# Kernel optimization log

Hardware: AMD Instinct MI355X
Metric: run time of the kernel (lower is better)

## Reference

```python
import jax, jax.numpy as jnp
import numpy as np

R_MAX = 1.0
BASIS_MASK = 0xFF        # low 8 bits -> basis index (basis_size=256)
R_BITS_MASK = 0xFFFF     # next 16 bits -> quantized radius
R_DENOM = 65535.0
INT8_DENOM = 127.0


def setup_inputs() -> dict:
    key = jax.random.key(0)
    k_x, k_c, k_b, k_r, k_s, k_bias = jax.random.split(key, 6)
    B, S, D_in, D_out, BASIS = 4, 2048, 4096, 4096, 256
    x = jax.random.normal(k_x, (B, S, D_in), dtype=jnp.float32)
    codes = jax.random.randint(k_c, (D_out,), 0, 16777216, dtype=jnp.int32)
    basis_table = jax.random.normal(k_b, (BASIS, D_in), dtype=jnp.float32)
    residual_q = jax.random.randint(k_r, (D_out, D_in), 0, 256, dtype=jnp.int32)
    residual_scales = jax.random.uniform(k_s, (D_out,), dtype=jnp.float32) * 0.05
    bias = jax.random.normal(k_bias, (D_out,), dtype=jnp.float32)
    return {"x": x, "codes": codes, "basis_table": basis_table,
            "residual_q": residual_q, "residual_scales": residual_scales,
            "bias": bias}


def decode_weight(codes, basis_table, residual_q, residual_scales):
    # Bitfield decode: low 8 bits = basis index, next 16 bits = quantized radius in [0, r_max].
    idx = codes & BASIS_MASK                                   # [O]
    r = ((codes >> 8) & R_BITS_MASK).astype(jnp.float32) / R_DENOM * R_MAX  # [O]
    base = r[:, None] * basis_table[idx]                       # [O, I]
    resid = (residual_q.astype(jnp.float32) - 128.0) / INT8_DENOM  # dequant int8 residual
    return base + residual_scales[:, None] * resid             # [O, I]


def reference(x, codes, basis_table, residual_q, residual_scales, bias):
    W = decode_weight(codes, basis_table, residual_q, residual_scales)  # [O, I]
    # y = x @ W^T + bias  (fused dequant-matmul in the original CUDA kernel)
    return jnp.einsum("bsi,oi->bso", x, W) + bias
```

## Files before the change

kernel.cpp:

```cpp
#include <hip/hip_runtime.h>


typedef __bf16 bf16x8 __attribute__((ext_vector_type(8)));
typedef float f32x4 __attribute__((ext_vector_type(4)));
typedef int i32x4 __attribute__((ext_vector_type(4)));
typedef unsigned short u16x8 __attribute__((ext_vector_type(8)));

__device__ __forceinline__ unsigned short f2bf(float f) {
    union { float f; unsigned int u; } c; c.f = f;
    unsigned int u = c.u;
    u += 0x7fffu + ((u >> 16) & 1u);
    return (unsigned short)(u >> 16);
}
__device__ __forceinline__ float bf2f(unsigned short h) {
    union { unsigned int u; float f; } c; c.u = ((unsigned int)h) << 16;
    return c.f;
}

__device__ __forceinline__ void load_lds16(const void* g, void* l) {
    __builtin_amdgcn_global_load_lds(
        (__attribute__((address_space(1))) void*)(void*)g,
        (__attribute__((address_space(3))) void*)l,
        16, 0, 0);
}

__device__ __forceinline__ int swz_decode(int p, int row_bytes) {
    const int g = p >> 3, t = p & 7, v = t ^ (g & 7);
    const int row = g * 2 + (v >> 2), chunk = v & 3;
    return row * row_bytes + chunk * 16;
}

__global__ void cvt_bf16_kernel(const float4* __restrict__ in4,
                                ushort4* __restrict__ out4, int n4) {
    int i = blockIdx.x * blockDim.x + threadIdx.x;
    const int stride = gridDim.x * blockDim.x;
    for (; i < n4; i += stride) {
        float4 v = in4[i];
        ushort4 o;
        o.x = f2bf(v.x); o.y = f2bf(v.y); o.z = f2bf(v.z); o.w = f2bf(v.w);
        out4[i] = o;
    }
}

__global__ void quant_x_kernel(const float* __restrict__ x,
                               signed char* __restrict__ xq,
                               float* __restrict__ arow, int K) {
    const int m = blockIdx.x;
    const float* row = x + (size_t)m * K;
    const int base = threadIdx.x * 16;
    float4 v[4];
#pragma unroll
    for (int j = 0; j < 4; ++j) v[j] = *(const float4*)(row + base + j * 4);

    float lmax = 0.f;
#pragma unroll
    for (int j = 0; j < 4; ++j) {
        lmax = fmaxf(lmax, fabsf(v[j].x));
        lmax = fmaxf(lmax, fabsf(v[j].y));
        lmax = fmaxf(lmax, fabsf(v[j].z));
        lmax = fmaxf(lmax, fabsf(v[j].w));
    }
#pragma unroll
    for (int off = 32; off; off >>= 1)
        lmax = fmaxf(lmax, __shfl_xor(lmax, off));
    __shared__ float smax[4];
    if ((threadIdx.x & 63) == 0) smax[threadIdx.x >> 6] = lmax;
    __syncthreads();
    const float mx = fmaxf(fmaxf(smax[0], smax[1]), fmaxf(smax[2], smax[3]));
    const float inv = mx > 0.f ? 127.0f / mx : 0.0f;
    if (threadIdx.x == 0) arow[m] = mx * (1.0f / 127.0f);

    union { signed char c[16]; i32x4 w; } pk;
#pragma unroll
    for (int j = 0; j < 4; ++j) {
        pk.c[j * 4 + 0] = (signed char)(int)rintf(v[j].x * inv);
        pk.c[j * 4 + 1] = (signed char)(int)rintf(v[j].y * inv);
        pk.c[j * 4 + 2] = (signed char)(int)rintf(v[j].z * inv);
        pk.c[j * 4 + 3] = (signed char)(int)rintf(v[j].w * inv);
    }
    *(i32x4*)(xq + (size_t)m * K + base) = pk.w;
}

__global__ void pack_q_kernel(const int4* __restrict__ q4,
                              unsigned int* __restrict__ out, int n4) {
    const int i = blockIdx.x * blockDim.x + threadIdx.x;
    if (i >= n4) return;
    int4 a = q4[i];
    unsigned int w = ((unsigned)(a.x - 128) & 0xFFu)
                   | (((unsigned)(a.y - 128) & 0xFFu) << 8)
                   | (((unsigned)(a.z - 128) & 0xFFu) << 16)
                   | (((unsigned)(a.w - 128) & 0xFFu) << 24);
    out[i] = w;
}

__global__ __launch_bounds__(512) void
p_gemm_kernel(const float* __restrict__ x,
              const unsigned short* __restrict__ Bb,
              unsigned short* __restrict__ Pbf,
              int M, int K) {
    __shared__ __align__(16) float As[2][32 * 64];
    __shared__ __align__(16) unsigned short Bs[2][256 * 64];

    const int tid  = threadIdx.x;
    const int lane = tid & 63;
    const int wv   = tid >> 6;
    const int wr   = wv >> 2;
    const int wc   = wv & 3;
    const int m0 = blockIdx.x * 32;
    const int lr = lane & 15;
    const int kg = lane >> 4;

    f32x4 acc[4];
#pragma unroll
    for (int ni = 0; ni < 4; ++ni) acc[ni] = (f32x4){0.f, 0.f, 0.f, 0.f};

    const int aRow = tid >> 4;
    const int aSrc = (tid & 15) ^ (aRow & 15);
    int bRow[4], bSrc[4];
#pragma unroll
    for (int j = 0; j < 4; ++j) {
        const int p = tid + 512 * j;
        bRow[j] = p >> 3;
        bSrc[j] = (p & 7) ^ (bRow[j] & 7);
    }
    const float* aG = x + (size_t)(m0 + aRow) * K + aSrc * 4;
    const unsigned short* bG[4];
#pragma unroll
    for (int j = 0; j < 4; ++j) bG[j] = Bb + (size_t)bRow[j] * K + bSrc[j] * 8;

#define P_STAGE(bb, k0)                                                        \
    do {                                                                       \
        load_lds16(aG + (k0), (char*)As[bb] + tid * 16);                       \
        _Pragma("unroll") for (int j = 0; j < 4; ++j)                          \
            load_lds16(bG[j] + (k0), (char*)Bs[bb] + (tid + 512 * j) * 16);    \
    } while (0)

    P_STAGE(0, 0);
    const int NT = K >> 6;
    for (int t = 0; t < NT; ++t) {
        const int bb = t & 1;
        if (t + 1 < NT) {
            P_STAGE(bb ^ 1, (t + 1) << 6);
            asm volatile("s_waitcnt vmcnt(5)" ::: "memory");
        } else {
            asm volatile("s_waitcnt vmcnt(0)" ::: "memory");
        }
        __builtin_amdgcn_s_barrier();

        const float* Ab = As[bb];
        const unsigned short* Bbf = Bs[bb];
#pragma unroll
        for (int s = 0; s < 2; ++s) {
            const int r = wr * 16 + lr;
            const int c0 = s * 8 + kg * 2;
            const int ph0 = c0 ^ (r & 15);
            const int ph1 = (c0 + 1) ^ (r & 15);
            f32x4 lo = *(const f32x4*)(Ab + r * 64 + ph0 * 4);
            f32x4 hi = *(const f32x4*)(Ab + r * 64 + ph1 * 4);
            bf16x8 a;
            a[0] = (__bf16)lo[0]; a[1] = (__bf16)lo[1];
            a[2] = (__bf16)lo[2]; a[3] = (__bf16)lo[3];
            a[4] = (__bf16)hi[0]; a[5] = (__bf16)hi[1];
            a[6] = (__bf16)hi[2]; a[7] = (__bf16)hi[3];
#pragma unroll
            for (int ni = 0; ni < 4; ++ni) {
                const int rb = wc * 64 + ni * 16 + lr;
                const int ph = (s * 4 + kg) ^ (rb & 7);
                bf16x8 bfr = __builtin_bit_cast(bf16x8,
                    *(const u16x8*)(Bbf + rb * 64 + ph * 8));
                acc[ni] = __builtin_amdgcn_mfma_f32_16x16x32_bf16(
                    a, bfr, acc[ni], 0, 0, 0);
            }
        }
        __builtin_amdgcn_s_barrier();
    }
#undef P_STAGE

#pragma unroll
    for (int ni = 0; ni < 4; ++ni) {
        const int n = wc * 64 + ni * 16 + lr;
        const int mb = m0 + wr * 16 + kg * 4;
#pragma unroll
        for (int rg = 0; rg < 4; ++rg)
            Pbf[(size_t)(mb + rg) * 256 + n] = f2bf(acc[ni][rg]);
    }
}

__global__ __launch_bounds__(256, 2) void
gemm_i8_kernel(const signed char* __restrict__ Xq,
               const signed char* __restrict__ Qb,
               const float* __restrict__ arow,
               const int* __restrict__ codes,
               const float* __restrict__ scales,
               const float* __restrict__ bias,
               const unsigned short* __restrict__ Pbf,
               float* __restrict__ out,
               int M, int N, int K) {
    __shared__ __align__(16) signed char As[2][128 * 64];
    __shared__ __align__(16) signed char Bs[2][256 * 64];

    const int tid  = threadIdx.x;
    const int lane = tid & 63;
    const int wv   = tid >> 6;
    const int wr   = wv >> 1;
    const int wc   = wv & 1;
    const int m0 = blockIdx.x * 128;
    const int n0 = blockIdx.y * 256;
    const int lr = lane & 15;
    const int kg = lane >> 4;
    const int cidx = (((lr & 1) << 2) | kg) ^ ((lr >> 1) & 7);

    i32x4 acc[4][8];
#pragma unroll
    for (int mi = 0; mi < 4; ++mi)
#pragma unroll
        for (int ni = 0; ni < 8; ++ni)
            acc[mi][ni] = (i32x4){0, 0, 0, 0};

    int gaOff[2], gbOff[4];
#pragma unroll
    for (int j = 0; j < 2; ++j) gaOff[j] = swz_decode(tid + 256 * j, 64);
#pragma unroll
    for (int j = 0; j < 4; ++j) gbOff[j] = swz_decode(tid + 256 * j, 64);

    const signed char* aSrc[2];
    const signed char* bSrc[4];
#pragma unroll
    for (int j = 0; j < 2; ++j)
        aSrc[j] = Xq + (size_t)(m0 + (gaOff[j] >> 6)) * K + (gaOff[j] & 63);
#pragma unroll
    for (int j = 0; j < 4; ++j)
        bSrc[j] = Qb + (size_t)(n0 + (gbOff[j] >> 6)) * K + (gbOff[j] & 63);

#define G_STAGE(bb, k0)                                                        \
    do {                                                                       \
        _Pragma("unroll") for (int j = 0; j < 2; ++j)                          \
            load_lds16(aSrc[j] + (k0), (char*)As[bb] + (tid + 256 * j) * 16);  \
        _Pragma("unroll") for (int j = 0; j < 4; ++j)                          \
            load_lds16(bSrc[j] + (k0), (char*)Bs[bb] + (tid + 256 * j) * 16);  \
    } while (0)

    G_STAGE(0, 0);
    asm volatile("s_waitcnt vmcnt(0)" ::: "memory");
    __builtin_amdgcn_s_barrier();

    const int NT = K >> 6;
#pragma unroll 2
    for (int t = 0; t < NT; ++t) {
        const int bb = t & 1;
        if (t + 1 < NT) G_STAGE(bb ^ 1, (t + 1) << 6);

        i32x4 af[4], bfr[8];
#pragma unroll
        for (int mi = 0; mi < 4; ++mi) {
            const int r2 = wr * 32 + mi * 8 + (lr >> 1);
            af[mi] = *(const i32x4*)(As[bb] + r2 * 128 + cidx * 16);
        }
#pragma unroll
        for (int ni = 0; ni < 8; ++ni) {
            const int r2 = wc * 64 + ni * 8 + (lr >> 1);
            bfr[ni] = *(const i32x4*)(Bs[bb] + r2 * 128 + cidx * 16);
        }
#pragma unroll
        for (int mi = 0; mi < 4; ++mi)
#pragma unroll
            for (int ni = 0; ni < 8; ++ni)
                acc[mi][ni] = __builtin_amdgcn_mfma_i32_16x16x64_i8(
                    af[mi], bfr[ni], acc[mi][ni], 0, 0, 0);

        asm volatile("s_waitcnt vmcnt(0)" ::: "memory");
        __builtin_amdgcn_s_barrier();
    }
#undef G_STAGE

    float av[4][4];
#pragma unroll
    for (int mi = 0; mi < 4; ++mi)
#pragma unroll
        for (int rg = 0; rg < 4; ++rg)
            av[mi][rg] = arow[m0 + wr * 64 + mi * 16 + kg * 4 + rg];

#pragma unroll
    for (int ni = 0; ni < 8; ++ni) {
        const int n = n0 + wc * 128 + ni * 16 + lr;
        const int code = codes[n];
        const int cc = code & 0xFF;
        const float rr = (float)((code >> 8) & 0xFFFF) * (1.0f / 65535.0f);
        const float so = scales[n] * (1.0f / 127.0f);
        const float bv = bias[n];
#pragma unroll
        for (int mi = 0; mi < 4; ++mi) {
            const int mbase = m0 + wr * 64 + mi * 16 + kg * 4;
            unsigned short pv[4];
#pragma unroll
            for (int rg = 0; rg < 4; ++rg)
                pv[rg] = Pbf[(size_t)(mbase + rg) * 256 + cc];
#pragma unroll
            for (int rg = 0; rg < 4; ++rg) {
                const float y = av[mi][rg] * so * (float)acc[mi][ni][rg]
                              + rr * bf2f(pv[rg]) + bv;
                __builtin_nontemporal_store(y, &out[(size_t)(mbase + rg) * N + n]);
            }
        }
    }
}

extern "C" void kernel_launch(void* const* d_in, const int* in_sizes, int n_in,
                              void* d_out, int out_size, void* d_ws, size_t ws_size,
                              hipStream_t stream) {
    const float* x        = (const float*)d_in[0];
    const int*   codes    = (const int*)d_in[1];
    const float* basis    = (const float*)d_in[2];
    const int*   q        = (const int*)d_in[3];
    const float* scales   = (const float*)d_in[4];
    const float* bias     = (const float*)d_in[5];
    float* out = (float*)d_out;

    const int BASIS = 256;
    const int K = in_sizes[2] / BASIS;
    const int N = in_sizes[1];
    const int M = in_sizes[0] / K;

    char* ws = (char*)d_ws;
    signed char* Xq = (signed char*)ws;
    size_t off = (size_t)M * K;
    signed char* Qb = (signed char*)(ws + off);
    off += (size_t)N * K;
    unsigned short* Pbf = (unsigned short*)(ws + off);
    off += (size_t)M * 256 * 2;
    float* Arow = (float*)(ws + off);
    off += (size_t)M * sizeof(float);
    unsigned short* Bb = (unsigned short*)(ws + off);

    cvt_bf16_kernel<<<1024, 256, 0, stream>>>((const float4*)basis, (ushort4*)Bb,
                                              BASIS * K / 4);
    p_gemm_kernel<<<M / 32, 512, 0, stream>>>(x, Bb, Pbf, M, K);
    quant_x_kernel<<<M, 256, 0, stream>>>(x, Xq, Arow, K);
    pack_q_kernel<<<(N * K / 4 + 255) / 256, 256, 0, stream>>>(
        (const int4*)q, (unsigned int*)Qb, N * K / 4);
    gemm_i8_kernel<<<dim3(M / 128, N / 256), 256, 0, stream>>>(
        Xq, Qb, Arow, codes, scales, bias, Pbf, out, M, N, K);
}
```

Baseline: 493.0 us.

## Fuse prep kernels into one launch and single-buffer the int8 GEMM main loop

Merges the bf16 basis conversion, the per-row x quantization and the residual packing into one prep kernel. Block IDs are interleaved so quantize and pack work share a launch, which removes two kernel launches and their tails. Separately, the int8 GEMM drops its LDS double buffering for a single buffer with two __syncthreads per K step. That halves LDS use, which could raise occupancy, but global loads no longer overlap with MFMA compute.

After: 496.7 us. Within noise of the previous version (+0.7%).

```diff
diff --git a/kernel.cpp b/kernel.cpp
--- a/kernel.cpp
+++ b/kernel.cpp
@@ -30,67 +30,90 @@
     return row * row_bytes + chunk * 16;
 }
 
-__global__ void cvt_bf16_kernel(const float4* __restrict__ in4,
-                                ushort4* __restrict__ out4, int n4) {
-    int i = blockIdx.x * blockDim.x + threadIdx.x;
-    const int stride = gridDim.x * blockDim.x;
-    for (; i < n4; i += stride) {
-        float4 v = in4[i];
-        ushort4 o;
-        o.x = f2bf(v.x); o.y = f2bf(v.y); o.z = f2bf(v.z); o.w = f2bf(v.w);
-        out4[i] = o;
-    }
-}
-
-__global__ void quant_x_kernel(const float* __restrict__ x,
-                               signed char* __restrict__ xq,
-                               float* __restrict__ arow, int K) {
-    const int m = blockIdx.x;
+__global__ __launch_bounds__(256) void
+prep_kernel(const float* __restrict__ x,
+            signed char* __restrict__ xq,
+            float* __restrict__ arow,
+            int M, int K,
+            const int4* __restrict__ q4,
+            unsigned int* __restrict__ qout,
+            int n4p,
+            const float4* __restrict__ b4,
+            ushort4* __restrict__ bb4,
+            int n4c) {
+    const int id = blockIdx.x;
+    const int tid = threadIdx.x;
+
+    if (id < 256) {
+#pragma unroll
+        for (int k = 0; k < 4; ++k) {
+            const int i = id * 1024 + k * 256 + tid;
+            if (i < n4c) {
+                float4 v = b4[i];
+                ushort4 o;
+                o.x = f2bf(v.x); o.y = f2bf(v.y);
+                o.z = f2bf(v.z); o.w = f2bf(v.w);
+                bb4[i] = o;
+            }
+        }
+        return;
+    }
+
+    const int j = id - 256;
+    const int g = j / 3;
+    const int r = j - g * 3;
+
+    if (r == 2) {
+#pragma unroll
+        for (int k = 0; k < 4; ++k) {
+            const int i = g * 1024 + k * 256 + tid;
+            if (i < n4p) {
+                int4 a = q4[i];
+                unsigned int w = ((unsigned)(a.x - 128) & 0xFFu)
+                               | (((unsigned)(a.y - 128) & 0xFFu) << 8)
+                               | (((unsigned)(a.z - 128) & 0xFFu) << 16)
+                               | (((unsigned)(a.w - 128) & 0xFFu) << 24);
+                qout[i] = w;
+            }
+        }
+        return;
+    }
+
+    const int m = g * 2 + r;
+    if (m >= M) return;
     const float* row = x + (size_t)m * K;
-    const int base = threadIdx.x * 16;
+    const int base = tid * 16;
     float4 v[4];
 #pragma unroll
-    for (int j = 0; j < 4; ++j) v[j] = *(const float4*)(row + base + j * 4);
+    for (int jj = 0; jj < 4; ++jj) v[jj] = *(const float4*)(row + base + jj * 4);
 
     float lmax = 0.f;
 #pragma unroll
-    for (int j = 0; j < 4; ++j) {
-        lmax = fmaxf(lmax, fabsf(v[j].x));
-        lmax = fmaxf(lmax, fabsf(v[j].y));
-        lmax = fmaxf(lmax, fabsf(v[j].z));
-        lmax = fmaxf(lmax, fabsf(v[j].w));
+    for (int jj = 0; jj < 4; ++jj) {
+        lmax = fmaxf(lmax, fabsf(v[jj].x));
+        lmax = fmaxf(lmax, fabsf(v[jj].y));
+        lmax = fmaxf(lmax, fabsf(v[jj].z));
+        lmax = fmaxf(lmax, fabsf(v[jj].w));
     }
 #pragma unroll
     for (int off = 32; off; off >>= 1)
         lmax = fmaxf(lmax, __shfl_xor(lmax, off));
     __shared__ float smax[4];
-    if ((threadIdx.x & 63) == 0) smax[threadIdx.x >> 6] = lmax;
+    if ((tid & 63) == 0) smax[tid >> 6] = lmax;
     __syncthreads();
     const float mx = fmaxf(fmaxf(smax[0], smax[1]), fmaxf(smax[2], smax[3]));
     const float inv = mx > 0.f ? 127.0f / mx : 0.0f;
-    if (threadIdx.x == 0) arow[m] = mx * (1.0f / 127.0f);
+    if (tid == 0) arow[m] = mx * (1.0f / 127.0f);
 
     union { signed char c[16]; i32x4 w; } pk;
 #pragma unroll
-    for (int j = 0; j < 4; ++j) {
-        pk.c[j * 4 + 0] = (signed char)(int)rintf(v[j].x * inv);
-        pk.c[j * 4 + 1] = (signed char)(int)rintf(v[j].y * inv);
-        pk.c[j * 4 + 2] = (signed char)(int)rintf(v[j].z * inv);
-        pk.c[j * 4 + 3] = (signed char)(int)rintf(v[j].w * inv);
+    for (int jj = 0; jj < 4; ++jj) {
+        pk.c[jj * 4 + 0] = (signed char)(int)rintf(v[jj].x * inv);
+        pk.c[jj * 4 + 1] = (signed char)(int)rintf(v[jj].y * inv);
+        pk.c[jj * 4 + 2] = (signed char)(int)rintf(v[jj].z * inv);
+        pk.c[jj * 4 + 3] = (signed char)(int)rintf(v[jj].w * inv);
     }
     *(i32x4*)(xq + (size_t)m * K + base) = pk.w;
-}
-
-__global__ void pack_q_kernel(const int4* __restrict__ q4,
-                              unsigned int* __restrict__ out, int n4) {
-    const int i = blockIdx.x * blockDim.x + threadIdx.x;
-    if (i >= n4) return;
-    int4 a = q4[i];
-    unsigned int w = ((unsigned)(a.x - 128) & 0xFFu)
-                   | (((unsigned)(a.y - 128) & 0xFFu) << 8)
-                   | (((unsigned)(a.z - 128) & 0xFFu) << 16)
-                   | (((unsigned)(a.w - 128) & 0xFFu) << 24);
-    out[i] = w;
 }
 
 __global__ __launch_bounds__(512) void
@@ -196,8 +219,8 @@
                const unsigned short* __restrict__ Pbf,
                float* __restrict__ out,
                int M, int N, int K) {
-    __shared__ __align__(16) signed char As[2][128 * 64];
-    __shared__ __align__(16) signed char Bs[2][256 * 64];
+    __shared__ __align__(16) signed char As[128 * 64];
+    __shared__ __align__(16) signed char Bs[256 * 64];
 
     const int tid  = threadIdx.x;
     const int lane = tid & 63;
@@ -223,43 +246,27 @@
 #pragma unroll
     for (int j = 0; j < 4; ++j) gbOff[j] = swz_decode(tid + 256 * j, 64);
 
-    const signed char* aSrc[2];
-    const signed char* bSrc[4];
-#pragma unroll
-    for (int j = 0; j < 2; ++j)
-        aSrc[j] = Xq + (size_t)(m0 + (gaOff[j] >> 6)) * K + (gaOff[j] & 63);
-#pragma unroll
-    for (int j = 0; j < 4; ++j)
-        bSrc[j] = Qb + (size_t)(n0 + (gbOff[j] >> 6)) * K + (gbOff[j] & 63);
-
-#define G_STAGE(bb, k0)                                                        \
-    do {                                                                       \
-        _Pragma("unroll") for (int j = 0; j < 2; ++j)                          \
-            load_lds16(aSrc[j] + (k0), (char*)As[bb] + (tid + 256 * j) * 16);  \
-        _Pragma("unroll") for (int j = 0; j < 4; ++j)                          \
-            load_lds16(bSrc[j] + (k0), (char*)Bs[bb] + (tid + 256 * j) * 16);  \
-    } while (0)
-
-    G_STAGE(0, 0);
-    asm volatile("s_waitcnt vmcnt(0)" ::: "memory");
-    __builtin_amdgcn_s_barrier();
-
-    const int NT = K >> 6;
-#pragma unroll 2
-    for (int t = 0; t < NT; ++t) {
-        const int bb = t & 1;
-        if (t + 1 < NT) G_STAGE(bb ^ 1, (t + 1) << 6);
+    for (int k0 = 0; k0 < K; k0 += 64) {
+#pragma unroll
+        for (int j = 0; j < 2; ++j)
+            load_lds16(Xq + (size_t)(m0 + (gaOff[j] >> 6)) * K + (gaOff[j] & 63) + k0,
+                       As + (tid + 256 * j) * 16);
+#pragma unroll
+        for (int j = 0; j < 4; ++j)
+            load_lds16(Qb + (size_t)(n0 + (gbOff[j] >> 6)) * K + (gbOff[j] & 63) + k0,
+                       Bs + (tid + 256 * j) * 16);
+        __syncthreads();
 
         i32x4 af[4], bfr[8];
 #pragma unroll
         for (int mi = 0; mi < 4; ++mi) {
             const int r2 = wr * 32 + mi * 8 + (lr >> 1);
-            af[mi] = *(const i32x4*)(As[bb] + r2 * 128 + cidx * 16);
+            af[mi] = *(const i32x4*)(As + r2 * 128 + cidx * 16);
         }
 #pragma unroll
         for (int ni = 0; ni < 8; ++ni) {
             const int r2 = wc * 64 + ni * 8 + (lr >> 1);
-            bfr[ni] = *(const i32x4*)(Bs[bb] + r2 * 128 + cidx * 16);
+            bfr[ni] = *(const i32x4*)(Bs + r2 * 128 + cidx * 16);
         }
 #pragma unroll
         for (int mi = 0; mi < 4; ++mi)
@@ -267,11 +274,8 @@
             for (int ni = 0; ni < 8; ++ni)
                 acc[mi][ni] = __builtin_amdgcn_mfma_i32_16x16x64_i8(
                     af[mi], bfr[ni], acc[mi][ni], 0, 0, 0);
-
-        asm volatile("s_waitcnt vmcnt(0)" ::: "memory");
-        __builtin_amdgcn_s_barrier();
-    }
-#undef G_STAGE
+        __syncthreads();
+    }
 
     float av[4][4];
 #pragma unroll
@@ -332,12 +336,17 @@
     off += (size_t)M * sizeof(float);
     unsigned short* Bb = (unsigned short*)(ws + off);
 
-    cvt_bf16_kernel<<<1024, 256, 0, stream>>>((const float4*)basis, (ushort4*)Bb,
-                                              BASIS * K / 4);
+    const int n4p = N * K / 4;
+    const int n4c = BASIS * K / 4;
+    const int g_quant = (M + 1) / 2;
+    const int g_pack  = (n4p + 1023) / 1024;
+    const int G3 = g_quant > g_pack ? g_quant : g_pack;
+    const int NB = 256 + 3 * G3;
+
+    prep_kernel<<<NB, 256, 0, stream>>>(x, Xq, Arow, M, K,
+                                        (const int4*)q, (unsigned int*)Qb, n4p,
+                                        (const float4*)basis, (ushort4*)Bb, n4c);
     p_gemm_kernel<<<M / 32, 512, 0, stream>>>(x, Bb, Pbf, M, K);
-    quant_x_kernel<<<M, 256, 0, stream>>>(x, Xq, Arow, K);
-    pack_q_kernel<<<(N * K / 4 + 255) / 256, 256, 0, stream>>>(
-        (const int4*)q, (unsigned int*)Qb, N * K / 4);
     gemm_i8_kernel<<<dim3(M / 128, N / 256), 256, 0, stream>>>(
         Xq, Qb, Arow, codes, scales, bias, Pbf, out, M, N, K);
 }
```
